# Performance work log

Measured on AMD Instinct MI355X. Metric: run time of the kernel, lower is better.

## Reference

```python
import jax, jax.numpy as jnp
import numpy as np

T = 4096          # tokens (batch*seq)
DIM = 2048        # model dim
INTER = 1024      # moe_inter_dim
E = 32            # n_routed_experts
TOPK = 6          # n_activated_experts
G = 8             # n_expert_groups
TOPK_G = 4        # n_limited_groups
SHARED_INTER = 2 * INTER  # n_shared_experts * moe_inter_dim
ROUTE_SCALE = 1.0


def setup_inputs() -> dict:
    key = jax.random.key(0)
    ks = jax.random.split(key, 8)
    s = 0.02
    return {
        "x": jax.random.normal(ks[0], (T, DIM), jnp.float32),
        "gate_w": jax.random.normal(ks[1], (E, DIM), jnp.float32) * s,
        "wg": jax.random.normal(ks[2], (E, DIM, INTER), jnp.float32) * s,   # gate_proj (stored [in,out])
        "wu": jax.random.normal(ks[3], (E, DIM, INTER), jnp.float32) * s,   # up_proj
        "wd": jax.random.normal(ks[4], (E, INTER, DIM), jnp.float32) * s,   # down_proj
        "swg": jax.random.normal(ks[5], (DIM, SHARED_INTER), jnp.float32) * s,
        "swu": jax.random.normal(ks[6], (DIM, SHARED_INTER), jnp.float32) * s,
        "swd": jax.random.normal(ks[7], (SHARED_INTER, DIM), jnp.float32) * s,
    }


def _gate(x, gate_w):
    # scores = softmax(x @ W^T); bias is None since dim != 7168 -> group score = amax
    scores = jax.nn.softmax(x @ gate_w.T, axis=-1)          # [T, E]
    orig = scores
    gs = scores.reshape(x.shape[0], G, E // G)              # [T, G, E/G]
    group_scores = gs.max(axis=-1)                          # [T, G]
    _, gidx = jax.lax.top_k(group_scores, TOPK_G)           # [T, TOPK_G]
    gmask = jnp.zeros((x.shape[0], G), bool).at[
        jnp.arange(x.shape[0])[:, None], gidx].set(True)
    masked = jnp.where(gmask[:, :, None], gs, -jnp.inf).reshape(x.shape[0], E)
    _, idx = jax.lax.top_k(masked, TOPK)                    # [T, TOPK]
    w = jnp.take_along_axis(orig, idx, axis=1) * ROUTE_SCALE  # softmax path: no renorm
    return w, idx


def reference(x, gate_w, wg, wu, wd, swg, swu, swd):
    weights, indices = _gate(x, gate_w)
    # combine[t, e] = routing weight of expert e for token t (0 if not selected)
    combine = (jax.nn.one_hot(indices, E, dtype=x.dtype) * weights[..., None]).sum(axis=1)  # [T, E]
    y = jnp.zeros_like(x)
    for e in range(E):  # fixed small loop over structurally distinct expert params
        h = jax.nn.silu(x @ wg[e]) * (x @ wu[e])            # [T, INTER]
        y = y + (h @ wd[e]) * combine[:, e:e + 1]
    shared = (jax.nn.silu(x @ swg) * (x @ swu)) @ swd       # shared experts MLP
    return y + shared
```

## Files before the change

### kernel.cpp

```cpp
#include <hip/hip_runtime.h>
#include <hip/hip_bf16.h>

typedef float f32x4 __attribute__((ext_vector_type(4)));
typedef __bf16 bf16x8 __attribute__((ext_vector_type(8)));
typedef unsigned short u16;

#define T_TOK 4096
#define DIMK 2048
#define INTERN 1024
#define NEXP 32
#define NTOPK 6
#define NGRP 8
#define NTOPG 4
#define SINTER 2048
#define MAXPADROWS 29184

__device__ __forceinline__ void glds16(const void* g, void* l) {
    auto* gp = (const __attribute__((address_space(1))) int*)(g);
    auto* lp = (__attribute__((address_space(3))) int*)(l);
    __builtin_amdgcn_global_load_lds(gp, lp, 16, 0, 0);
}

__device__ __forceinline__ size_t toff(int row, int k, int K) {
    int g = (k >> 3) & 7;
    return (size_t)(row >> 7) * (size_t)(128 * K) + (size_t)(k >> 6) * 8192 +
           (size_t)((row & 127) * 64 + ((g ^ (row & 7)) << 3) + (k & 7));
}

__global__ __launch_bounds__(256) void cast_x_tiled_kernel(const float* __restrict__ in, u16* __restrict__ out) {
    int gi = (blockIdx.x * 256 + threadIdx.x) * 8;
    int row = gi >> 11, k = gi & 2047;
    const float4* p = reinterpret_cast<const float4*>(in + gi);
    float4 a = p[0], b = p[1];
    bf16x8 v;
    v[0] = (__bf16)a.x; v[1] = (__bf16)a.y; v[2] = (__bf16)a.z; v[3] = (__bf16)a.w;
    v[4] = (__bf16)b.x; v[5] = (__bf16)b.y; v[6] = (__bf16)b.z; v[7] = (__bf16)b.w;
    *reinterpret_cast<bf16x8*>(out + toff(row, k, DIMK)) = v;
}

template <int KD, int JD>
__global__ __launch_bounds__(256) void trans_tiled_kernel(const float* __restrict__ in, u16* __restrict__ out) {
    __shared__ float tile[64 * 65];
    const int t = threadIdx.x;
    const float* ib = in + (size_t)blockIdx.z * KD * JD;
    u16* ob = out + (size_t)blockIdx.z * KD * JD;
    const int j0 = blockIdx.x * 64, k0 = blockIdx.y * 64;
    {
        const int c4 = (t & 15) * 4;
#pragma unroll
        for (int i = 0; i < 4; ++i) {
            const int r = (t >> 4) + i * 16;
            float4 v = *reinterpret_cast<const float4*>(&ib[(size_t)(k0 + r) * JD + j0 + c4]);
            tile[r * 65 + c4 + 0] = v.x;
            tile[r * 65 + c4 + 1] = v.y;
            tile[r * 65 + c4 + 2] = v.z;
            tile[r * 65 + c4 + 3] = v.w;
        }
    }
    __syncthreads();
    {
        const int jl = t >> 2, kh = (t & 3) * 16;
        const int n = j0 + jl;
        bf16x8 v0, v1;
#pragma unroll
        for (int j = 0; j < 8; ++j) v0[j] = (__bf16)tile[(kh + j) * 65 + jl];
#pragma unroll
        for (int j = 0; j < 8; ++j) v1[j] = (__bf16)tile[(kh + 8 + j) * 65 + jl];
        *reinterpret_cast<bf16x8*>(ob + toff(n, k0 + kh, KD)) = v0;
        *reinterpret_cast<bf16x8*>(ob + toff(n, k0 + kh + 8, KD)) = v1;
    }
}

template <int KD, int JD>
__global__ __launch_bounds__(256) void cat_trans_kernel(const float* __restrict__ g0, const float* __restrict__ u0,
                                                        u16* __restrict__ out) {
    __shared__ float tile[64 * 65];
    const int t = threadIdx.x;
    const size_t so = (size_t)blockIdx.z * KD * JD;
    u16* ob = out + (size_t)blockIdx.z * (2 * (size_t)KD * JD);
    const int j0 = blockIdx.x * 32, k0 = blockIdx.y * 64;
    const int kl = t >> 2, jf = (t & 3) * 4;
#pragma unroll
    for (int s = 0; s < 2; ++s) {
        const float* src = (s ? u0 : g0) + so;
#pragma unroll
        for (int rep = 0; rep < 2; ++rep) {
            int jb = jf + rep * 16;
            float4 v = *reinterpret_cast<const float4*>(&src[(size_t)(k0 + kl) * JD + j0 + jb]);
            int nl = ((jb >> 4) << 5) + s * 16 + (jb & 15);
            tile[kl * 65 + nl + 0] = v.x;
            tile[kl * 65 + nl + 1] = v.y;
            tile[kl * 65 + nl + 2] = v.z;
            tile[kl * 65 + nl + 3] = v.w;
        }
    }
    __syncthreads();
    {
        const int nl = t >> 2, kh = (t & 3) * 16;
        const int n = 2 * j0 + nl;
        bf16x8 v0, v1;
#pragma unroll
        for (int j = 0; j < 8; ++j) v0[j] = (__bf16)tile[(kh + j) * 65 + nl];
#pragma unroll
        for (int j = 0; j < 8; ++j) v1[j] = (__bf16)tile[(kh + 8 + j) * 65 + nl];
        *reinterpret_cast<bf16x8*>(ob + toff(n, k0 + kh, KD)) = v0;
        *reinterpret_cast<bf16x8*>(ob + toff(n, k0 + kh + 8, KD)) = v1;
    }
}

__global__ __launch_bounds__(64) void gate_kernel(const float* __restrict__ x, const float* __restrict__ gw,
                                                  int* __restrict__ counts, int* __restrict__ ids,
                                                  int* __restrict__ tok2row, float* __restrict__ wtok) {
    const int t = blockIdx.x;
    const int lane = threadIdx.x;
    __shared__ float logits[NEXP];
    const float4* xr = reinterpret_cast<const float4*>(x + (size_t)t * DIMK);
    for (int e = 0; e < NEXP; ++e) {
        const float4* gr = reinterpret_cast<const float4*>(gw + (size_t)e * DIMK);
        float acc = 0.f;
#pragma unroll
        for (int i = 0; i < DIMK / 4 / 64; ++i) {
            float4 xv = xr[lane + i * 64];
            float4 gv = gr[lane + i * 64];
            acc += xv.x * gv.x + xv.y * gv.y + xv.z * gv.z + xv.w * gv.w;
        }
#pragma unroll
        for (int s = 32; s; s >>= 1) acc += __shfl_xor(acc, s);
        if (lane == 0) logits[e] = acc;
    }
    if (lane != 0) return;
    float sc[NEXP];
#pragma unroll
    for (int e = 0; e < NEXP; ++e) sc[e] = logits[e];
    float mx = sc[0];
#pragma unroll
    for (int e = 1; e < NEXP; ++e) mx = fmaxf(mx, sc[e]);
    float ssum = 0.f;
#pragma unroll
    for (int e = 0; e < NEXP; ++e) { sc[e] = __expf(sc[e] - mx); ssum += sc[e]; }
    const float inv = 1.f / ssum;
    float gsc[NGRP];
#pragma unroll
    for (int g = 0; g < NGRP; ++g) {
        float m2 = sc[g * 4];
#pragma unroll
        for (int j = 1; j < 4; ++j) m2 = fmaxf(m2, sc[g * 4 + j]);
        gsc[g] = m2;
    }
    int gsel = 0;
    for (int r = 0; r < NTOPG; ++r) {
        float bv = -1.f; int bi = 0;
#pragma unroll
        for (int g = 0; g < NGRP; ++g) {
            bool c = (((gsel >> g) & 1) == 0) && (gsc[g] > bv);
            bv = c ? gsc[g] : bv; bi = c ? g : bi;
        }
        gsel |= (1 << bi);
    }
    float msk[NEXP];
#pragma unroll
    for (int e = 0; e < NEXP; ++e) msk[e] = ((gsel >> (e >> 2)) & 1) ? sc[e] : -1.f;
    for (int r = 0; r < NTOPK; ++r) {
        float bv = -3.f; int bi = 0;
#pragma unroll
        for (int e = 0; e < NEXP; ++e) {
            bool c = msk[e] > bv;
            bv = c ? msk[e] : bv; bi = c ? e : bi;
        }
#pragma unroll
        for (int e = 0; e < NEXP; ++e) if (e == bi) msk[e] = -2.f;
        float w = bv * inv;
        int slot = atomicAdd(&counts[bi], 1);
        ids[bi * T_TOK + slot] = t;
        tok2row[t * NTOPK + r] = (bi << 12) | slot;
        wtok[t * NTOPK + r] = w;
    }
}

__global__ void scan_kernel(const int* __restrict__ counts, int* __restrict__ poff) {
    if (threadIdx.x == 0) {
        int o = 0;
        for (int e = 0; e < NEXP; ++e) { poff[e] = o; o += (counts[e] + 127) & ~127; }
    }
}


__global__ __launch_bounds__(512, 2) void gemm1_fused_kernel(
    const u16* __restrict__ xbT, const u16* __restrict__ WcatE, u16* __restrict__ H,
    const u16* __restrict__ WcatS, u16* __restrict__ Hs,
    const int* __restrict__ counts, const int* __restrict__ poff, const int* __restrict__ ids) {
    __shared__ u16 Alds[2 * 16384];
    __shared__ u16 Blds[3 * 16384];
    constexpr int NT = DIMK / 64;

    int bm, bn, M, Mpad, hbase, HKdim, e = 0;
    const u16* b0;
    u16* ho;
    bool gath;
    if (blockIdx.z < 32) {
        int lin = blockIdx.x + 16 * (blockIdx.y + 8 * blockIdx.z);
        e = 31 - (((lin >> 10) << 3) | (lin & 7));
        int j = (lin >> 3) & 127;
        bm = j & 15; bn = j >> 4;
        M = counts[e];
        if (bm * 256 >= M) return;
        Mpad = (M + 127) & ~127;
        hbase = poff[e];
        b0 = WcatE + (size_t)e * 2048 * DIMK;
        ho = H; HKdim = INTERN; gath = true;
    } else {
        int lin = blockIdx.x + 16 * (blockIdx.y + 8 * (blockIdx.z - 32));
        int swz = (lin & 7) * 32 + (lin >> 3);
        bm = swz & 15; bn = swz >> 4;
        M = T_TOK; Mpad = T_TOK; hbase = 0;
        b0 = WcatS; ho = Hs; HKdim = SINTER; gath = false;
    }

    const int tid = threadIdx.x;
    const int t8 = tid * 8;
    size_t aSrc[2][2];
#pragma unroll
    for (int h = 0; h < 2; ++h)
#pragma unroll
        for (int j = 0; j < 2; ++j) {
            int drow = j * 64 + (tid >> 3);
            int row = bm * 256 + h * 128 + drow;
            int tok;
            if (gath) { int cr = row < M ? row : M - 1; tok = ids[e * T_TOK + cr]; }
            else tok = row;
            int slot = (tid & 7) ^ (drow & 7) ^ (tok & 7);
            aSrc[h][j] = (size_t)(tok >> 7) * (size_t)(128 * 2048) + (size_t)((tok & 127) * 64 + slot * 8);
        }
    const u16* bCh[2] = { b0 + (size_t)(2 * bn + 0) * (128 * 2048), b0 + (size_t)(2 * bn + 1) * (128 * 2048) };

    const int lane = tid & 63, wv = tid >> 6;
    const int wr = wv >> 2, wc = wv & 3;
    const int l15 = lane & 15, lk = lane >> 4;

    f32x4 acc[8][4];
#pragma unroll
    for (int m = 0; m < 8; ++m)
#pragma unroll
        for (int n = 0; n < 4; ++n) acc[m][n] = {0.f, 0.f, 0.f, 0.f};

    auto SA = [&](int kt, int h, int buf) {
        glds16(xbT + aSrc[h][0] + (size_t)kt * 8192, &Alds[buf * 16384 + h * 8192 + t8]);
        glds16(xbT + aSrc[h][1] + (size_t)kt * 8192, &Alds[buf * 16384 + h * 8192 + 4096 + t8]);
    };
    auto SB = [&](int kt, int h, int buf) {
        glds16(bCh[h] + (size_t)kt * 8192 + t8, &Blds[buf * 16384 + h * 8192 + t8]);
        glds16(bCh[h] + (size_t)kt * 8192 + 4096 + t8, &Blds[buf * 16384 + h * 8192 + 4096 + t8]);
    };
    bf16x8 afr[4][2], bfr0[2][2], bfr1[2][2];
    auto DSRA = [&](int buf, int mh) {
#pragma unroll
        for (int mi = 0; mi < 4; ++mi)
#pragma unroll
            for (int ki = 0; ki < 2; ++ki) {
                int rl = wr * 128 + mh * 64 + mi * 16 + l15;
                int g = ki * 4 + lk;
                afr[mi][ki] = *reinterpret_cast<const bf16x8*>(
                    &Alds[buf * 16384 + (rl >> 7) * 8192 + (rl & 127) * 64 + ((g ^ (rl & 7)) << 3)]);
            }
    };
    auto DSRB = [&](int buf, int nh, bf16x8 (&bf)[2][2]) {
#pragma unroll
        for (int nj = 0; nj < 2; ++nj)
#pragma unroll
            for (int ki = 0; ki < 2; ++ki) {
                int rc = wc * 64 + (nh * 2 + nj) * 16 + l15;
                int g = ki * 4 + lk;
                bf[nj][ki] = *reinterpret_cast<const bf16x8*>(
                    &Blds[buf * 16384 + (rc >> 7) * 8192 + (rc & 127) * 64 + ((g ^ (rc & 7)) << 3)]);
            }
    };

    SA(0, 0, 0); SA(0, 1, 0);
    SB(0, 0, 0); SB(0, 1, 0);
    SB(1, 0, 1); SB(1, 1, 1);
    asm volatile("s_waitcnt vmcnt(4)" ::: "memory");
    __builtin_amdgcn_s_barrier();

#pragma unroll 1
    for (int t = 0; t < NT; ++t) {
        const int abuf = t & 1;
        const int bbuf = t % 3;
        const int b3 = (t + 2) % 3;
        DSRA(abuf, 0);
        DSRB(bbuf, 0, bfr0);
        if (t + 1 < NT) { SA(t + 1, 0, abuf ^ 1); SA(t + 1, 1, abuf ^ 1); }
        __builtin_amdgcn_s_barrier();
        __builtin_amdgcn_s_setprio(1);
#pragma unroll
        for (int ki = 0; ki < 2; ++ki)
#pragma unroll
            for (int mi = 0; mi < 4; ++mi)
#pragma unroll
                for (int nj = 0; nj < 2; ++nj)
                    acc[mi][nj] = __builtin_amdgcn_mfma_f32_16x16x32_bf16(afr[mi][ki], bfr0[nj][ki], acc[mi][nj], 0, 0, 0);
        __builtin_amdgcn_s_setprio(0);
        __builtin_amdgcn_s_barrier();
        DSRB(bbuf, 1, bfr1);
        if (t + 2 < NT) SB(t + 2, 0, b3);
        __builtin_amdgcn_s_barrier();
        __builtin_amdgcn_s_setprio(1);
#pragma unroll
        for (int ki = 0; ki < 2; ++ki)
#pragma unroll
            for (int mi = 0; mi < 4; ++mi)
#pragma unroll
                for (int nj = 0; nj < 2; ++nj)
                    acc[mi][2 + nj] = __builtin_amdgcn_mfma_f32_16x16x32_bf16(afr[mi][ki], bfr1[nj][ki], acc[mi][2 + nj], 0, 0, 0);
        __builtin_amdgcn_s_setprio(0);
        __builtin_amdgcn_s_barrier();
        DSRA(abuf, 1);
        if (t + 2 < NT) SB(t + 2, 1, b3);
        __builtin_amdgcn_s_barrier();
        __builtin_amdgcn_s_setprio(1);
#pragma unroll
        for (int ki = 0; ki < 2; ++ki)
#pragma unroll
            for (int mi = 0; mi < 4; ++mi)
#pragma unroll
                for (int nj = 0; nj < 2; ++nj)
                    acc[4 + mi][2 + nj] = __builtin_amdgcn_mfma_f32_16x16x32_bf16(afr[mi][ki], bfr1[nj][ki], acc[4 + mi][2 + nj], 0, 0, 0);
        __builtin_amdgcn_s_setprio(0);
        __builtin_amdgcn_s_barrier();
        __builtin_amdgcn_s_setprio(1);
#pragma unroll
        for (int ki = 0; ki < 2; ++ki)
#pragma unroll
            for (int mi = 0; mi < 4; ++mi)
#pragma unroll
                for (int nj = 0; nj < 2; ++nj)
                    acc[4 + mi][nj] = __builtin_amdgcn_mfma_f32_16x16x32_bf16(afr[mi][ki], bfr0[nj][ki], acc[4 + mi][nj], 0, 0, 0);
        __builtin_amdgcn_s_setprio(0);
        if (t + 2 < NT) { asm volatile("s_waitcnt vmcnt(4)" ::: "memory"); }
        else { asm volatile("s_waitcnt vmcnt(0)" ::: "memory"); }
        __builtin_amdgcn_s_barrier();
    }

#pragma unroll
    for (int mI = 0; mI < 8; ++mI) {
#pragma unroll
        for (int r = 0; r < 4; ++r) {
            int grow = bm * 256 + wr * 128 + mI * 16 + lk * 4 + r;
            if (grow < Mpad) {
#pragma unroll
                for (int nh = 0; nh < 2; ++nh) {
                    float gg = acc[mI][nh * 2 + 0][r];
                    float uu = acc[mI][nh * 2 + 1][r];
                    float h = gg / (1.f + __expf(-gg)) * uu;
                    int n = bn * 256 + wc * 64 + nh * 32 + l15;
                    int jcol = ((n >> 5) << 4) + (n & 15);
                    __bf16 hb = (__bf16)h;
                    ho[toff(hbase + grow, jcol, HKdim)] = __builtin_bit_cast(u16, hb);
                }
            }
        }
    }
}

__global__ __launch_bounds__(512, 2) void gemm2_fused_kernel(
    const u16* __restrict__ H, const u16* __restrict__ wdT, u16* __restrict__ Ye,
    const u16* __restrict__ Hs, const u16* __restrict__ swdT, u16* __restrict__ Yss,
    const int* __restrict__ counts, const int* __restrict__ poff) {
    __shared__ u16 Alds[2 * 16384];
    __shared__ u16 Blds[3 * 16384];
    constexpr int NT = 16;

    int bm, bn, M, rowbase, AKK, kt0;
    const u16 *aBase, *bBase;
    u16* yo;
    if (blockIdx.z < 32) {
        int lin = blockIdx.x + 16 * (blockIdx.y + 8 * blockIdx.z);
        int e = 31 - (((lin >> 10) << 3) | (lin & 7));
        int j = (lin >> 3) & 127;
        bm = j & 15; bn = j >> 4;
        M = counts[e];
        if (bm * 256 >= M) return;
        rowbase = poff[e];
        aBase = H + (size_t)poff[e] * INTERN;
        bBase = wdT + (size_t)e * 2048 * INTERN;
        yo = Ye; AKK = INTERN; kt0 = 0;
    } else {
        int lin = blockIdx.x + 16 * (blockIdx.y + 8 * (blockIdx.z - 32));
        int swz = (lin & 7) * 32 + (lin >> 3);
        bm = swz & 15; bn = (swz >> 4) & 7;
        int ks = swz >> 7;
        M = T_TOK; rowbase = ks * T_TOK;
        aBase = Hs; bBase = swdT; yo = Yss; AKK = SINTER; kt0 = ks * 16;
    }
    const u16* aCh[2] = { aBase + (size_t)(2 * bm + 0) * (size_t)(128 * AKK) + (size_t)kt0 * 8192,
                          aBase + (size_t)(2 * bm + 1) * (size_t)(128 * AKK) + (size_t)kt0 * 8192 };
    const u16* bCh[2] = { bBase + (size_t)(2 * bn + 0) * (size_t)(128 * AKK) + (size_t)kt0 * 8192,
                          bBase + (size_t)(2 * bn + 1) * (size_t)(128 * AKK) + (size_t)kt0 * 8192 };
    const int tid = threadIdx.x;
    const int t8 = tid * 8;
    const int lane = tid & 63, wv = tid >> 6;
    const int wr = wv >> 2, wc = wv & 3;
    const int l15 = lane & 15, lk = lane >> 4;

    f32x4 acc[8][4];
#pragma unroll
    for (int m = 0; m < 8; ++m)
#pragma unroll
        for (int n = 0; n < 4; ++n) acc[m][n] = {0.f, 0.f, 0.f, 0.f};

    auto SA = [&](int kt, int h, int buf) {
        glds16(aCh[h] + (size_t)kt * 8192 + t8, &Alds[buf * 16384 + h * 8192 + t8]);
        glds16(aCh[h] + (size_t)kt * 8192 + 4096 + t8, &Alds[buf * 16384 + h * 8192 + 4096 + t8]);
    };
    auto SB = [&](int kt, int h, int buf) {
        glds16(bCh[h] + (size_t)kt * 8192 + t8, &Blds[buf * 16384 + h * 8192 + t8]);
        glds16(bCh[h] + (size_t)kt * 8192 + 4096 + t8, &Blds[buf * 16384 + h * 8192 + 4096 + t8]);
    };
    bf16x8 afr[4][2], bfr0[2][2], bfr1[2][2];
    auto DSRA = [&](int buf, int mh) {
#pragma unroll
        for (int mi = 0; mi < 4; ++mi)
#pragma unroll
            for (int ki = 0; ki < 2; ++ki) {
                int rl = wr * 128 + mh * 64 + mi * 16 + l15;
                int g = ki * 4 + lk;
                afr[mi][ki] = *reinterpret_cast<const bf16x8*>(
                    &Alds[buf * 16384 + (rl >> 7) * 8192 + (rl & 127) * 64 + ((g ^ (rl & 7)) << 3)]);
            }
    };
    auto DSRB = [&](int buf, int nh, bf16x8 (&bf)[2][2]) {
#pragma unroll
        for (int nj = 0; nj < 2; ++nj)
#pragma unroll
            for (int ki = 0; ki < 2; ++ki) {
                int rc = wc * 64 + (nh * 2 + nj) * 16 + l15;
                int g = ki * 4 + lk;
                bf[nj][ki] = *reinterpret_cast<const bf16x8*>(
                    &Blds[buf * 16384 + (rc >> 7) * 8192 + (rc & 127) * 64 + ((g ^ (rc & 7)) << 3)]);
            }
    };

    SA(0, 0, 0); SA(0, 1, 0);
    SB(0, 0, 0); SB(0, 1, 0);
    SB(1, 0, 1); SB(1, 1, 1);
    asm volatile("s_waitcnt vmcnt(4)" ::: "memory");
    __builtin_amdgcn_s_barrier();

#pragma unroll 1
    for (int t = 0; t < NT; ++t) {
        const int abuf = t & 1;
        const int bbuf = t % 3;
        const int b3 = (t + 2) % 3;
        DSRA(abuf, 0);
        DSRB(bbuf, 0, bfr0);
        if (t + 1 < NT) { SA(t + 1, 0, abuf ^ 1); SA(t + 1, 1, abuf ^ 1); }
        __builtin_amdgcn_s_barrier();
        __builtin_amdgcn_s_setprio(1);
#pragma unroll
        for (int ki = 0; ki < 2; ++ki)
#pragma unroll
            for (int mi = 0; mi < 4; ++mi)
#pragma unroll
                for (int nj = 0; nj < 2; ++nj)
                    acc[mi][nj] = __builtin_amdgcn_mfma_f32_16x16x32_bf16(afr[mi][ki], bfr0[nj][ki], acc[mi][nj], 0, 0, 0);
        __builtin_amdgcn_s_setprio(0);
        __builtin_amdgcn_s_barrier();
        DSRB(bbuf, 1, bfr1);
        if (t + 2 < NT) SB(t + 2, 0, b3);
        __builtin_amdgcn_s_barrier();
        __builtin_amdgcn_s_setprio(1);
#pragma unroll
        for (int ki = 0; ki < 2; ++ki)
#pragma unroll
            for (int mi = 0; mi < 4; ++mi)
#pragma unroll
                for (int nj = 0; nj < 2; ++nj)
                    acc[mi][2 + nj] = __builtin_amdgcn_mfma_f32_16x16x32_bf16(afr[mi][ki], bfr1[nj][ki], acc[mi][2 + nj], 0, 0, 0);
        __builtin_amdgcn_s_setprio(0);
        __builtin_amdgcn_s_barrier();
        DSRA(abuf, 1);
        if (t + 2 < NT) SB(t + 2, 1, b3);
        __builtin_amdgcn_s_barrier();
        __builtin_amdgcn_s_setprio(1);
#pragma unroll
        for (int ki = 0; ki < 2; ++ki)
#pragma unroll
            for (int mi = 0; mi < 4; ++mi)
#pragma unroll
                for (int nj = 0; nj < 2; ++nj)
                    acc[4 + mi][2 + nj] = __builtin_amdgcn_mfma_f32_16x16x32_bf16(afr[mi][ki], bfr1[nj][ki], acc[4 + mi][2 + nj], 0, 0, 0);
        __builtin_amdgcn_s_setprio(0);
        __builtin_amdgcn_s_barrier();
        __builtin_amdgcn_s_setprio(1);
#pragma unroll
        for (int ki = 0; ki < 2; ++ki)
#pragma unroll
            for (int mi = 0; mi < 4; ++mi)
#pragma unroll
                for (int nj = 0; nj < 2; ++nj)
                    acc[4 + mi][nj] = __builtin_amdgcn_mfma_f32_16x16x32_bf16(afr[mi][ki], bfr0[nj][ki], acc[4 + mi][nj], 0, 0, 0);
        __builtin_amdgcn_s_setprio(0);
        if (t + 2 < NT) { asm volatile("s_waitcnt vmcnt(4)" ::: "memory"); }
        else { asm volatile("s_waitcnt vmcnt(0)" ::: "memory"); }
        __builtin_amdgcn_s_barrier();
    }

#pragma unroll
    for (int mI = 0; mI < 8; ++mI) {
#pragma unroll
        for (int r = 0; r < 4; ++r) {
            int grow = bm * 256 + wr * 128 + mI * 16 + lk * 4 + r;
            if (grow < M) {
                u16* yr = yo + (size_t)(rowbase + grow) * 2048;
#pragma unroll
                for (int ni = 0; ni < 4; ++ni) {
                    int col = bn * 256 + wc * 64 + ni * 16 + l15;
                    __bf16 yb = (__bf16)acc[mI][ni][r];
                    yr[col] = __builtin_bit_cast(u16, yb);
                }
            }
        }
    }
}

__global__ __launch_bounds__(256) void combine_kernel(const u16* __restrict__ Yss, const u16* __restrict__ Ye,
                                                      const int* __restrict__ tok2row, const float* __restrict__ wtok,
                                                      const int* __restrict__ poff, float* __restrict__ out) {
    const int t = blockIdx.x;
    const int c = threadIdx.x * 8;
    bf16x8 v0 = *reinterpret_cast<const bf16x8*>(Yss + (size_t)t * 2048 + c);
    bf16x8 v1 = *reinterpret_cast<const bf16x8*>(Yss + (size_t)(T_TOK + t) * 2048 + c);
    float acc[8];
#pragma unroll
    for (int j = 0; j < 8; ++j) acc[j] = (float)v0[j] + (float)v1[j];
#pragma unroll
    for (int r = 0; r < NTOPK; ++r) {
        int pk = tok2row[t * NTOPK + r];
        int e = pk >> 12, sl = pk & 4095;
        int row = poff[e] + sl;
        float w = wtok[t * NTOPK + r];
        bf16x8 v = *reinterpret_cast<const bf16x8*>(Ye + (size_t)row * 2048 + c);
#pragma unroll
        for (int j = 0; j < 8; ++j) acc[j] += w * (float)v[j];
    }
    float4 o0 = {acc[0], acc[1], acc[2], acc[3]};
    float4 o1 = {acc[4], acc[5], acc[6], acc[7]};
    float4* po = reinterpret_cast<float4*>(out + (size_t)t * 2048 + c);
    po[0] = o0; po[1] = o1;
}

extern "C" void kernel_launch(void* const* d_in, const int* in_sizes, int n_in,
                              void* d_out, int out_size, void* d_ws, size_t ws_size,
                              hipStream_t stream) {
    const float* x = (const float*)d_in[0];
    const float* gate_w = (const float*)d_in[1];
    const float* wg = (const float*)d_in[2];
    const float* wu = (const float*)d_in[3];
    const float* wd = (const float*)d_in[4];
    const float* swg = (const float*)d_in[5];
    const float* swu = (const float*)d_in[6];
    const float* swd = (const float*)d_in[7];
    float* out = (float*)d_out;

    char* ws = (char*)d_ws;
    size_t off = 0;
    auto alloc = [&](size_t bytes) {
        void* p = ws + off;
        off = (off + bytes + 255) & ~(size_t)255;
        return p;
    };
    u16* xbT = (u16*)alloc((size_t)T_TOK * DIMK * 2);
    u16* H = (u16*)alloc((size_t)MAXPADROWS * INTERN * 2);
    u16* Hs = (u16*)alloc((size_t)T_TOK * SINTER * 2);
    u16* Ye = (u16*)alloc((size_t)MAXPADROWS * 2048 * 2);
    u16* Yss = (u16*)alloc((size_t)2 * T_TOK * 2048 * 2);
    int* ids = (int*)alloc((size_t)NEXP * T_TOK * 4);
    int* tok2row = (int*)alloc((size_t)T_TOK * NTOPK * 4);
    float* wtok = (float*)alloc((size_t)T_TOK * NTOPK * 4);
    int* counts = (int*)alloc(NEXP * 4);
    int* poff = (int*)alloc(NEXP * 4);
    u16* WcatS = (u16*)alloc((size_t)(2 * SINTER) * DIMK * 2);
    u16* swdT = (u16*)alloc((size_t)DIMK * SINTER * 2);
    u16* WcatE = (u16*)alloc((size_t)NEXP * (2 * INTERN) * DIMK * 2);
    u16* wdT = WcatE;

    hipMemsetAsync(counts, 0, NEXP * 4, stream);
    cast_x_tiled_kernel<<<(T_TOK * DIMK) / (256 * 8), 256, 0, stream>>>(x, xbT);
    gate_kernel<<<T_TOK, 64, 0, stream>>>(x, gate_w, counts, ids, tok2row, wtok);
    scan_kernel<<<1, 64, 0, stream>>>(counts, poff);

    cat_trans_kernel<DIMK, SINTER><<<dim3(SINTER / 32, DIMK / 64, 1), 256, 0, stream>>>(swg, swu, WcatS);
    cat_trans_kernel<DIMK, INTERN><<<dim3(INTERN / 32, DIMK / 64, NEXP), 256, 0, stream>>>(wg, wu, WcatE);
    trans_tiled_kernel<SINTER, DIMK><<<dim3(DIMK / 64, SINTER / 64, 1), 256, 0, stream>>>(swd, swdT);

    gemm1_fused_kernel<<<dim3(16, 8, 34), 512, 0, stream>>>(
        xbT, WcatE, H, WcatS, Hs, counts, poff, ids);

    trans_tiled_kernel<INTERN, DIMK><<<dim3(DIMK / 64, INTERN / 64, NEXP), 256, 0, stream>>>(wd, wdT);

    gemm2_fused_kernel<<<dim3(16, 8, 34), 512, 0, stream>>>(
        H, wdT, Ye, Hs, swdT, Yss, counts, poff);

    combine_kernel<<<T_TOK, 256, 0, stream>>>(Yss, Ye, tok2row, wtok, poff, out);
}
```

Measured before the change: 1.006 ms.

## Interleave weight transposes with GEMM blocks in fused launches to overlap work

Restructures the launch schedule so that the expert weight transpose/cast tiles run in the same kernels as the GEMMs. The shared-expert GEMM1 runs alongside the expert gate/up transposes, and the expert GEMM1 and shared GEMM2 run alongside the down-proj transpose. The separate gemm kernels become device functions dispatched by a linear block index. This aims to hide the memory-bound fp32-to-bf16 transposes behind compute-bound MFMA work and to cut the number of serialized phases. In exchange it needs extra workspace for a separate wdT buffer, and it mixes block types with different resource use inside one launch.

```diff
diff --git a/kernel.cpp b/kernel.cpp
--- a/kernel.cpp
+++ b/kernel.cpp
@@ -38,73 +38,27 @@
     *reinterpret_cast<bf16x8*>(out + toff(row, k, DIMK)) = v;
 }
 
-template <int KD, int JD>
-__global__ __launch_bounds__(256) void trans_tiled_kernel(const float* __restrict__ in, u16* __restrict__ out) {
-    __shared__ float tile[64 * 65];
-    const int t = threadIdx.x;
-    const float* ib = in + (size_t)blockIdx.z * KD * JD;
-    u16* ob = out + (size_t)blockIdx.z * KD * JD;
-    const int j0 = blockIdx.x * 64, k0 = blockIdx.y * 64;
+template <bool CAT>
+__device__ __forceinline__ void tile_trans_512(const float* __restrict__ src, int JD, int k0, int j0,
+                                               u16* __restrict__ ob, int KOUT, int s, float* tile) {
+    const int tid = threadIdx.x;
     {
-        const int c4 = (t & 15) * 4;
-#pragma unroll
-        for (int i = 0; i < 4; ++i) {
-            const int r = (t >> 4) + i * 16;
-            float4 v = *reinterpret_cast<const float4*>(&ib[(size_t)(k0 + r) * JD + j0 + c4]);
-            tile[r * 65 + c4 + 0] = v.x;
-            tile[r * 65 + c4 + 1] = v.y;
-            tile[r * 65 + c4 + 2] = v.z;
-            tile[r * 65 + c4 + 3] = v.w;
-        }
+        const int r = tid >> 3, c8 = (tid & 7) * 8;
+        float4 v0 = *reinterpret_cast<const float4*>(&src[(size_t)(k0 + r) * JD + j0 + c8]);
+        float4 v1 = *reinterpret_cast<const float4*>(&src[(size_t)(k0 + r) * JD + j0 + c8 + 4]);
+        float* tp = &tile[r * 65 + c8];
+        tp[0] = v0.x; tp[1] = v0.y; tp[2] = v0.z; tp[3] = v0.w;
+        tp[4] = v1.x; tp[5] = v1.y; tp[6] = v1.z; tp[7] = v1.w;
     }
     __syncthreads();
     {
-        const int jl = t >> 2, kh = (t & 3) * 16;
-        const int n = j0 + jl;
-        bf16x8 v0, v1;
-#pragma unroll
-        for (int j = 0; j < 8; ++j) v0[j] = (__bf16)tile[(kh + j) * 65 + jl];
-#pragma unroll
-        for (int j = 0; j < 8; ++j) v1[j] = (__bf16)tile[(kh + 8 + j) * 65 + jl];
-        *reinterpret_cast<bf16x8*>(ob + toff(n, k0 + kh, KD)) = v0;
-        *reinterpret_cast<bf16x8*>(ob + toff(n, k0 + kh + 8, KD)) = v1;
-    }
-}
-
-template <int KD, int JD>
-__global__ __launch_bounds__(256) void cat_trans_kernel(const float* __restrict__ g0, const float* __restrict__ u0,
-                                                        u16* __restrict__ out) {
-    __shared__ float tile[64 * 65];
-    const int t = threadIdx.x;
-    const size_t so = (size_t)blockIdx.z * KD * JD;
-    u16* ob = out + (size_t)blockIdx.z * (2 * (size_t)KD * JD);
-    const int j0 = blockIdx.x * 32, k0 = blockIdx.y * 64;
-    const int kl = t >> 2, jf = (t & 3) * 4;
-#pragma unroll
-    for (int s = 0; s < 2; ++s) {
-        const float* src = (s ? u0 : g0) + so;
-#pragma unroll
-        for (int rep = 0; rep < 2; ++rep) {
-            int jb = jf + rep * 16;
-            float4 v = *reinterpret_cast<const float4*>(&src[(size_t)(k0 + kl) * JD + j0 + jb]);
-            int nl = ((jb >> 4) << 5) + s * 16 + (jb & 15);
-            tile[kl * 65 + nl + 0] = v.x;
-            tile[kl * 65 + nl + 1] = v.y;
-            tile[kl * 65 + nl + 2] = v.z;
-            tile[kl * 65 + nl + 3] = v.w;
-        }
-    }
-    __syncthreads();
-    {
-        const int nl = t >> 2, kh = (t & 3) * 16;
-        const int n = 2 * j0 + nl;
-        bf16x8 v0, v1;
-#pragma unroll
-        for (int j = 0; j < 8; ++j) v0[j] = (__bf16)tile[(kh + j) * 65 + nl];
-#pragma unroll
-        for (int j = 0; j < 8; ++j) v1[j] = (__bf16)tile[(kh + 8 + j) * 65 + nl];
-        *reinterpret_cast<bf16x8*>(ob + toff(n, k0 + kh, KD)) = v0;
-        *reinterpret_cast<bf16x8*>(ob + toff(n, k0 + kh + 8, KD)) = v1;
+        const int jl = tid >> 3, kh = (tid & 7) * 8;
+        const int j = j0 + jl;
+        const int n = CAT ? (((j >> 4) << 5) + s * 16 + (j & 15)) : j;
+        bf16x8 o;
+#pragma unroll
+        for (int jj = 0; jj < 8; ++jj) o[jj] = (__bf16)tile[(kh + jj) * 65 + jl];
+        *reinterpret_cast<bf16x8*>(ob + toff(n, k0 + kh, KOUT)) = o;
     }
 }
 
@@ -184,38 +138,12 @@
     }
 }
 
-
-__global__ __launch_bounds__(512, 2) void gemm1_fused_kernel(
-    const u16* __restrict__ xbT, const u16* __restrict__ WcatE, u16* __restrict__ H,
-    const u16* __restrict__ WcatS, u16* __restrict__ Hs,
-    const int* __restrict__ counts, const int* __restrict__ poff, const int* __restrict__ ids) {
-    __shared__ u16 Alds[2 * 16384];
-    __shared__ u16 Blds[3 * 16384];
+__device__ __forceinline__ void dev_gemm1(u16* smem, const u16* __restrict__ xbT, const u16* __restrict__ b0,
+                                          u16* __restrict__ ho, int bm, int bn, int M, int Mpad, int hbase,
+                                          int HKdim, bool gath, int e, const int* __restrict__ ids) {
+    u16* Alds = smem;
+    u16* Blds = smem + 32768;
     constexpr int NT = DIMK / 64;
-
-    int bm, bn, M, Mpad, hbase, HKdim, e = 0;
-    const u16* b0;
-    u16* ho;
-    bool gath;
-    if (blockIdx.z < 32) {
-        int lin = blockIdx.x + 16 * (blockIdx.y + 8 * blockIdx.z);
-        e = 31 - (((lin >> 10) << 3) | (lin & 7));
-        int j = (lin >> 3) & 127;
-        bm = j & 15; bn = j >> 4;
-        M = counts[e];
-        if (bm * 256 >= M) return;
-        Mpad = (M + 127) & ~127;
-        hbase = poff[e];
-        b0 = WcatE + (size_t)e * 2048 * DIMK;
-        ho = H; HKdim = INTERN; gath = true;
-    } else {
-        int lin = blockIdx.x + 16 * (blockIdx.y + 8 * (blockIdx.z - 32));
-        int swz = (lin & 7) * 32 + (lin >> 3);
-        bm = swz & 15; bn = swz >> 4;
-        M = T_TOK; Mpad = T_TOK; hbase = 0;
-        b0 = WcatS; ho = Hs; HKdim = SINTER; gath = false;
-    }
-
     const int tid = threadIdx.x;
     const int t8 = tid * 8;
     size_t aSrc[2][2];
@@ -361,36 +289,11 @@
     }
 }
 
-__global__ __launch_bounds__(512, 2) void gemm2_fused_kernel(
-    const u16* __restrict__ H, const u16* __restrict__ wdT, u16* __restrict__ Ye,
-    const u16* __restrict__ Hs, const u16* __restrict__ swdT, u16* __restrict__ Yss,
-    const int* __restrict__ counts, const int* __restrict__ poff) {
-    __shared__ u16 Alds[2 * 16384];
-    __shared__ u16 Blds[3 * 16384];
+__device__ __forceinline__ void dev_gemm2(u16* smem, const u16* __restrict__ aBase, const u16* __restrict__ bBase,
+                                          u16* __restrict__ yo, int bm, int bn, int M, int rowbase, int AKK, int kt0) {
+    u16* Alds = smem;
+    u16* Blds = smem + 32768;
     constexpr int NT = 16;
-
-    int bm, bn, M, rowbase, AKK, kt0;
-    const u16 *aBase, *bBase;
-    u16* yo;
-    if (blockIdx.z < 32) {
-        int lin = blockIdx.x + 16 * (blockIdx.y + 8 * blockIdx.z);
-        int e = 31 - (((lin >> 10) << 3) | (lin & 7));
-        int j = (lin >> 3) & 127;
-        bm = j & 15; bn = j >> 4;
-        M = counts[e];
-        if (bm * 256 >= M) return;
-        rowbase = poff[e];
-        aBase = H + (size_t)poff[e] * INTERN;
-        bBase = wdT + (size_t)e * 2048 * INTERN;
-        yo = Ye; AKK = INTERN; kt0 = 0;
-    } else {
-        int lin = blockIdx.x + 16 * (blockIdx.y + 8 * (blockIdx.z - 32));
-        int swz = (lin & 7) * 32 + (lin >> 3);
-        bm = swz & 15; bn = (swz >> 4) & 7;
-        int ks = swz >> 7;
-        M = T_TOK; rowbase = ks * T_TOK;
-        aBase = Hs; bBase = swdT; yo = Yss; AKK = SINTER; kt0 = ks * 16;
-    }
     const u16* aCh[2] = { aBase + (size_t)(2 * bm + 0) * (size_t)(128 * AKK) + (size_t)kt0 * 8192,
                           aBase + (size_t)(2 * bm + 1) * (size_t)(128 * AKK) + (size_t)kt0 * 8192 };
     const u16* bCh[2] = { bBase + (size_t)(2 * bn + 0) * (size_t)(128 * AKK) + (size_t)kt0 * 8192,
@@ -520,6 +423,99 @@
             }
         }
     }
+}
+
+__global__ __launch_bounds__(512, 2) void p0_trans_kernel(const float* __restrict__ swg, const float* __restrict__ swu,
+                                                          const float* __restrict__ swd,
+                                                          u16* __restrict__ WcatS, u16* __restrict__ swdT) {
+    __shared__ float tile[64 * 65];
+    int lin = blockIdx.x;
+    if (lin < 2048) {
+        int s = lin >> 10, v = lin & 1023;
+        int kt = (v >> 5) & 31, jt = v & 31;
+        tile_trans_512<true>((s ? swu : swg), SINTER, kt * 64, jt * 64, WcatS, DIMK, s, tile);
+    } else {
+        int v = lin - 2048;
+        int kt = v >> 5, jt = v & 31;
+        tile_trans_512<false>(swd, DIMK, kt * 64, jt * 64, swdT, SINTER, 0, tile);
+    }
+}
+
+__global__ __launch_bounds__(512, 2) void d1_kernel(const u16* __restrict__ xbT, const u16* __restrict__ WcatS,
+                                                    u16* __restrict__ Hs,
+                                                    const float* __restrict__ wg, const float* __restrict__ wu,
+                                                    u16* __restrict__ WcatE) {
+    __shared__ u16 smem[81920];
+    int lin = blockIdx.x;
+    int t = lin / 129, r = lin % 129;
+    if (r == 0) {
+        int swz = (t & 7) * 32 + (t >> 3);
+        int bm = swz & 15, bn = swz >> 4;
+        dev_gemm1(smem, xbT, WcatS, Hs, bm, bn, T_TOK, T_TOK, 0, SINTER, false, 0, nullptr);
+    } else {
+        int u = t * 128 + (r - 1);
+        int e = u >> 10, v = u & 1023;
+        int s = (v >> 9) & 1, kt = (v >> 4) & 31, jt = v & 15;
+        const float* src = (s ? wu : wg) + (size_t)e * DIMK * INTERN;
+        u16* ob = WcatE + (size_t)e * 2048 * DIMK;
+        tile_trans_512<true>(src, INTERN, kt * 64, jt * 64, ob, DIMK, s, (float*)smem);
+    }
+}
+
+__global__ __launch_bounds__(512, 2) void d2_kernel(const u16* __restrict__ xbT, const u16* __restrict__ WcatE,
+                                                    u16* __restrict__ H,
+                                                    const u16* __restrict__ Hs, const u16* __restrict__ swdT,
+                                                    u16* __restrict__ Yss,
+                                                    const float* __restrict__ wd, u16* __restrict__ wdTout,
+                                                    const int* __restrict__ counts, const int* __restrict__ poff,
+                                                    const int* __restrict__ ids) {
+    __shared__ u16 smem[81920];
+    int lin = blockIdx.x;
+    if (lin < 4352) {
+        int t = lin / 17, r = lin % 17;
+        if (r == 16) {
+            int swz = (t & 7) * 32 + (t >> 3);
+            int bm = swz & 15, bn = (swz >> 4) & 7, ks = swz >> 7;
+            dev_gemm2(smem, Hs, swdT, Yss, bm, bn, T_TOK, ks * T_TOK, SINTER, ks * 16);
+        } else {
+            int u = t * 16 + r;
+            int e = 31 - (((u >> 10) << 3) | (u & 7));
+            int j = (u >> 3) & 127;
+            int bm = j & 15, bn = j >> 4;
+            int M = counts[e];
+            if (bm * 256 >= M) return;
+            dev_gemm1(smem, xbT, WcatE + (size_t)e * 2048 * DIMK, H,
+                      bm, bn, M, (M + 127) & ~127, poff[e], INTERN, true, e, ids);
+        }
+    } else {
+        int u = lin - 4352;
+        int e = u >> 9, v = u & 511;
+        int kt = v >> 5, jt = v & 31;
+        tile_trans_512<false>(wd + (size_t)e * INTERN * DIMK, DIMK, kt * 64, jt * 64,
+                              wdTout + (size_t)e * DIMK * INTERN, INTERN, 0, (float*)smem);
+    }
+}
+
+__global__ __launch_bounds__(512, 2) void wdt_kernel(const float* __restrict__ wd, u16* __restrict__ wdTout) {
+    __shared__ float tile[64 * 65];
+    int u = blockIdx.x;
+    int e = u >> 9, v = u & 511;
+    tile_trans_512<false>(wd + (size_t)e * INTERN * DIMK, DIMK, (v >> 5) * 64, (v & 31) * 64,
+                          wdTout + (size_t)e * DIMK * INTERN, INTERN, 0, tile);
+}
+
+__global__ __launch_bounds__(512, 2) void d3_kernel(const u16* __restrict__ H, const u16* __restrict__ wdTu,
+                                                    u16* __restrict__ Ye,
+                                                    const int* __restrict__ counts, const int* __restrict__ poff) {
+    __shared__ u16 smem[81920];
+    int u = blockIdx.x;
+    int e = 31 - (((u >> 10) << 3) | (u & 7));
+    int j = (u >> 3) & 127;
+    int bm = j & 15, bn = j >> 4;
+    int M = counts[e];
+    if (bm * 256 >= M) return;
+    dev_gemm2(smem, H + (size_t)poff[e] * INTERN, wdTu + (size_t)e * 2048 * INTERN, Ye,
+              bm, bn, M, poff[e], INTERN, 0);
 }
 
 __global__ __launch_bounds__(256) void combine_kernel(const u16* __restrict__ Yss, const u16* __restrict__ Ye,
@@ -581,24 +577,26 @@
     u16* WcatS = (u16*)alloc((size_t)(2 * SINTER) * DIMK * 2);
     u16* swdT = (u16*)alloc((size_t)DIMK * SINTER * 2);
     u16* WcatE = (u16*)alloc((size_t)NEXP * (2 * INTERN) * DIMK * 2);
-    u16* wdT = WcatE;
+    u16* wdT2 = (u16*)alloc((size_t)NEXP * INTERN * DIMK * 2);
+    const bool wdFused = (off <= ws_size);
+    u16* wdTuse = wdFused ? wdT2 : WcatE;
 
     hipMemsetAsync(counts, 0, NEXP * 4, stream);
     cast_x_tiled_kernel<<<(T_TOK * DIMK) / (256 * 8), 256, 0, stream>>>(x, xbT);
     gate_kernel<<<T_TOK, 64, 0, stream>>>(x, gate_w, counts, ids, tok2row, wtok);
     scan_kernel<<<1, 64, 0, stream>>>(counts, poff);
 
-    cat_trans_kernel<DIMK, SINTER><<<dim3(SINTER / 32, DIMK / 64, 1), 256, 0, stream>>>(swg, swu, WcatS);
-    cat_trans_kernel<DIMK, INTERN><<<dim3(INTERN / 32, DIMK / 64, NEXP), 256, 0, stream>>>(wg, wu, WcatE);
-    trans_tiled_kernel<SINTER, DIMK><<<dim3(DIMK / 64, SINTER / 64, 1), 256, 0, stream>>>(swd, swdT);
-
-    gemm1_fused_kernel<<<dim3(16, 8, 34), 512, 0, stream>>>(
-        xbT, WcatE, H, WcatS, Hs, counts, poff, ids);
-
-    trans_tiled_kernel<INTERN, DIMK><<<dim3(DIMK / 64, INTERN / 64, NEXP), 256, 0, stream>>>(wd, wdT);
-
-    gemm2_fused_kernel<<<dim3(16, 8, 34), 512, 0, stream>>>(
-        H, wdT, Ye, Hs, swdT, Yss, counts, poff);
+    p0_trans_kernel<<<3072, 512, 0, stream>>>(swg, swu, swd, WcatS, swdT);
+
+    d1_kernel<<<33024, 512, 0, stream>>>(xbT, WcatS, Hs, wg, wu, WcatE);
+
+    d2_kernel<<<wdFused ? (4352 + 16384) : 4352, 512, 0, stream>>>(
+        xbT, WcatE, H, Hs, swdT, Yss, wd, wdTuse, counts, poff, ids);
+
+    if (!wdFused)
+        wdt_kernel<<<16384, 512, 0, stream>>>(wd, wdTuse);
+
+    d3_kernel<<<4096, 512, 0, stream>>>(H, wdTuse, Ye, counts, poff);
 
     combine_kernel<<<T_TOK, 256, 0, stream>>>(Yss, Ye, tok2row, wtok, poff, out);
 }
```

New measurement: 1.007 ms. No clear change (+0.0%).
